# Kernel tuning notes

Measured on AMD Instinct MI355X. Metric: run time of the kernel, lower is better.

The kernel has to match this reference:

```python
import jax, jax.numpy as jnp
import numpy as np

N_NODES = 50000


def setup_inputs() -> dict:
    key = jax.random.key(0)
    k1, k2, k3, k4, k5 = jax.random.split(key, 5)
    feature = jax.random.normal(k1, (N_NODES, 128), dtype=jnp.float32)
    src = jax.random.randint(k2, (1600000,), 0, N_NODES, dtype=jnp.int32)
    dst = jax.random.randint(k3, (1600000,), 0, N_NODES, dtype=jnp.int32)
    W = jax.random.normal(k4, (128, 128), dtype=jnp.float32) * (1.0 / np.sqrt(128))
    b = jax.random.normal(k5, (128,), dtype=jnp.float32) * 0.01
    return {"feature": feature, "src": src, "dst": dst, "W": W, "b": b}


def reference(feature, src, dst, W, b):
    # DGL update_all(copy_src('h','m'), sum('m','h')):
    # for each edge (u -> v): message m = h[u]; node v accumulates sum of incoming messages.
    msgs = feature[src]  # [E, F] gather
    h = jax.ops.segment_sum(msgs, dst, num_segments=N_NODES)  # [N, F] scatter-add
    # nn.Linear(in_feats, out_feats): h @ W.T + b
    return h @ W.T + b
```

## Files before the change

### kernel.cpp

```cpp
#include <hip/hip_runtime.h>

#define F      128
#define RSH    5
#define RNODES 32
#define NBUCK  1563
#define CB     1280
#define CH     4096
#define OVCAP  65536
#define G_PART 391

typedef __attribute__((ext_vector_type(8))) short short8;
typedef __attribute__((ext_vector_type(4))) float f32x4;

__device__ inline short f2bf(float f) {
  unsigned u = __float_as_uint(f);
  u += 0x7fff + ((u >> 16) & 1);
  return (short)(u >> 16);
}
__device__ inline float bf2f(unsigned short u) {
  return __uint_as_float((unsigned)u << 16);
}

__global__ __launch_bounds__(512) void k_fused(
    const float* __restrict__ X, const float* __restrict__ W,
    const int* __restrict__ src, const int* __restrict__ dst,
    unsigned short* __restrict__ Yb,
    unsigned* __restrict__ pk, unsigned* __restrict__ gcur,
    unsigned* __restrict__ ovcnt, unsigned long long* __restrict__ ovlist,
    int N, int E, int nTiles) {
  __shared__ unsigned smem[CH + 3 * NBUCK];
  const int t = threadIdx.x;

  if (blockIdx.x < G_PART) {
    unsigned* lpk   = smem;
    unsigned* cnt   = smem + CH;
    unsigned* offs  = cnt + NBUCK;
    unsigned* cur   = offs + NBUCK;
    const int nchunk = (E + CH - 1) / CH;

    for (int c = blockIdx.x; c < nchunk; c += G_PART) {
      const int e0   = c * CH;
      const int ecnt = min(CH, E - e0);

      for (int i = t; i < NBUCK; i += 512) cnt[i] = 0;
      __syncthreads();

      for (int i = t; i < ecnt; i += 512)
        atomicAdd(&cnt[(unsigned)dst[e0 + i] >> RSH], 1u);
      __syncthreads();

      unsigned lv0, lv1, lv2, lv3;
      {
        const int i0 = t * 4;
        lv0 = (i0 + 0 < NBUCK) ? cnt[i0 + 0] : 0;
        lv1 = (i0 + 1 < NBUCK) ? cnt[i0 + 1] : 0;
        lv2 = (i0 + 2 < NBUCK) ? cnt[i0 + 2] : 0;
        lv3 = (i0 + 3 < NBUCK) ? cnt[i0 + 3] : 0;
      }
      cur[t] = lv0 + lv1 + lv2 + lv3;
      __syncthreads();
      for (int d2 = 1; d2 < 512; d2 <<= 1) {
        const unsigned add = (t >= d2) ? cur[t - d2] : 0;
        __syncthreads();
        cur[t] += add;
        __syncthreads();
      }
      unsigned ebase = (t > 0) ? cur[t - 1] : 0;
      __syncthreads();
      {
        const int i0 = t * 4;
        if (i0 + 0 < NBUCK) { offs[i0 + 0] = ebase; cur[i0 + 0] = ebase; ebase += lv0; }
        if (i0 + 1 < NBUCK) { offs[i0 + 1] = ebase; cur[i0 + 1] = ebase; ebase += lv1; }
        if (i0 + 2 < NBUCK) { offs[i0 + 2] = ebase; cur[i0 + 2] = ebase; ebase += lv2; }
        if (i0 + 3 < NBUCK) { offs[i0 + 3] = ebase; cur[i0 + 3] = ebase; ebase += lv3; }
      }
      __syncthreads();

      for (int i = t; i < ecnt; i += 512) {
        const unsigned d = (unsigned)dst[e0 + i];
        const unsigned b = d >> RSH;
        const unsigned p = atomicAdd(&cur[b], 1u);
        lpk[p] = (unsigned)src[e0 + i] | ((d & (RNODES - 1)) << 16) | (b << 21);
      }
      __syncthreads();

      for (int i = t; i < NBUCK; i += 512) {
        const unsigned c0 = cnt[i];
        if (c0 > 0) cnt[i] = (unsigned)i * CB + atomicAdd(&gcur[i], c0);
      }
      __syncthreads();

      for (int p = t; p < ecnt; p += 512) {
        const unsigned v = lpk[p];
        const unsigned b = v >> 21;
        const unsigned idx = cnt[b] + ((unsigned)p - offs[b]);
        if (idx < (b + 1) * (unsigned)CB) {
          pk[idx] = v & 0x1FFFFFu;
        } else {
          const unsigned o = atomicAdd(ovcnt, 1u);
          if (o < OVCAP) {
            const unsigned s  = v & 0xFFFFu;
            const unsigned dl = (v >> 16) & (RNODES - 1);
            ovlist[o] = ((unsigned long long)(b * RNODES + dl) << 32) | s;
          }
        }
      }
      __syncthreads();
    }
  } else {
    short* Wp = (short*)smem;
    for (int fid = t; fid < 2048; fid += 512) {
      const int lane = fid & 63;
      const int c    = (fid >> 6) & 3;
      const int jt   = fid >> 8;
      const int j    = jt * 16 + (lane & 15);
      const int k0   = c * 32 + (lane >> 4) * 8;
      short8 s;
      #pragma unroll
      for (int i = 0; i < 8; ++i) s[i] = f2bf(W[j * F + k0 + i]);
      *reinterpret_cast<short8*>(Wp + fid * 8) = s;
    }
    __syncthreads();

    const int lane = t & 63;
    const int tile = (blockIdx.x - G_PART) * 8 + (t >> 6);
    if (tile >= nTiles) return;
    const int row0 = tile * 16;
    const int r    = row0 + (lane & 15);
    const int k0   = (lane >> 4) * 8;

    short8 a[4];
    #pragma unroll
    for (int c = 0; c < 4; ++c) {
      if (r < N) {
        const float* p = X + (size_t)r * F + c * 32 + k0;
        const float4 x0 = *reinterpret_cast<const float4*>(p);
        const float4 x1 = *reinterpret_cast<const float4*>(p + 4);
        a[c][0] = f2bf(x0.x); a[c][1] = f2bf(x0.y);
        a[c][2] = f2bf(x0.z); a[c][3] = f2bf(x0.w);
        a[c][4] = f2bf(x1.x); a[c][5] = f2bf(x1.y);
        a[c][6] = f2bf(x1.z); a[c][7] = f2bf(x1.w);
      } else {
        #pragma unroll
        for (int i = 0; i < 8; ++i) a[c][i] = 0;
      }
    }

    #pragma unroll
    for (int jt = 0; jt < 8; ++jt) {
      f32x4 acc = {0.f, 0.f, 0.f, 0.f};
      #pragma unroll
      for (int c = 0; c < 4; ++c) {
        const short8 bfrag = *reinterpret_cast<const short8*>(
            Wp + ((jt * 4 + c) * 64 + lane) * 8);
        acc = __builtin_amdgcn_mfma_f32_16x16x32_bf16(a[c], bfrag, acc, 0, 0, 0);
      }
      const int col   = jt * 16 + (lane & 15);
      const int rbase = row0 + (lane >> 4) * 4;
      #pragma unroll
      for (int reg = 0; reg < 4; ++reg)
        if (rbase + reg < N)
          Yb[(size_t)(rbase + reg) * F + col] = (unsigned short)f2bf(acc[reg]);
    }
  }
}

__global__ __launch_bounds__(512) void k_reduce2(
    const unsigned short* __restrict__ Yb,
    const unsigned* __restrict__ pk,
    const unsigned* __restrict__ gcur,
    const float* __restrict__ b,
    float* __restrict__ out,
    int N) {
  __shared__ unsigned s_pk[CB];
  __shared__ unsigned short s_src[CB];
  __shared__ unsigned lcnt[RNODES], loffs[RNODES], lcur[RNODES];
  const int bkt = blockIdx.x % NBUCK;
  const int s   = blockIdx.x / NBUCK;
  const int t = threadIdx.x;
  const unsigned base = (unsigned)bkt * CB;
  const unsigned m = min(gcur[bkt], (unsigned)CB);

  for (unsigned i = t; i < m; i += 512) s_pk[i] = pk[base + i];
  if (t < RNODES) lcnt[t] = 0;
  __syncthreads();
  for (unsigned i = t; i < m; i += 512)
    atomicAdd(&lcnt[s_pk[i] >> 16], 1u);
  __syncthreads();
  if (t == 0) {
    unsigned r = 0;
    #pragma unroll
    for (int i = 0; i < RNODES; ++i) { loffs[i] = r; lcur[i] = r; r += lcnt[i]; }
  }
  __syncthreads();
  for (unsigned i = t; i < m; i += 512) {
    const unsigned v = s_pk[i];
    const unsigned p = atomicAdd(&lcur[v >> 16], 1u);
    s_src[p] = (unsigned short)(v & 0xFFFFu);
  }
  __syncthreads();

  const int lane = t & 63;
  const int g    = lane >> 4;
  const int q    = lane & 15;
  const int dl   = (t >> 6) * 4 + g;
  const int v    = bkt * RNODES + dl;
  const int deg  = (int)lcnt[dl];
  const int off  = (int)loffs[dl];
  const unsigned short* Yh = Yb + s * 64;

  float acc[4];
  #pragma unroll
  for (int j = 0; j < 4; ++j) acc[j] = 0.f;

  int k = 0;
  for (; k + 3 < deg; k += 4) {
    int sid[4];
    #pragma unroll
    for (int u = 0; u < 4; ++u) sid[u] = (int)s_src[off + k + u];
    ushort4 y[4];
    #pragma unroll
    for (int u = 0; u < 4; ++u)
      y[u] = *reinterpret_cast<const ushort4*>(
          Yh + (size_t)sid[u] * F + q * 4);
    acc[0] += (bf2f(y[0].x) + bf2f(y[1].x)) + (bf2f(y[2].x) + bf2f(y[3].x));
    acc[1] += (bf2f(y[0].y) + bf2f(y[1].y)) + (bf2f(y[2].y) + bf2f(y[3].y));
    acc[2] += (bf2f(y[0].z) + bf2f(y[1].z)) + (bf2f(y[2].z) + bf2f(y[3].z));
    acc[3] += (bf2f(y[0].w) + bf2f(y[1].w)) + (bf2f(y[2].w) + bf2f(y[3].w));
  }
  for (; k < deg; ++k) {
    const int s0 = (int)s_src[off + k];
    const ushort4 y = *reinterpret_cast<const ushort4*>(
        Yh + (size_t)s0 * F + q * 4);
    acc[0] += bf2f(y.x); acc[1] += bf2f(y.y);
    acc[2] += bf2f(y.z); acc[3] += bf2f(y.w);
  }

  if (v < N) {
    const int j = s * 64 + q * 4;
    const float4 bb = *reinterpret_cast<const float4*>(b + j);
    float4 o = make_float4(acc[0] + bb.x, acc[1] + bb.y,
                           acc[2] + bb.z, acc[3] + bb.w);
    *reinterpret_cast<float4*>(out + (size_t)v * F + j) = o;
  }
}

__global__ __launch_bounds__(256) void k_overflow(
    const unsigned* __restrict__ ovcnt,
    const unsigned long long* __restrict__ ovlist,
    const unsigned short* __restrict__ Yb,
    float* __restrict__ out, int N) {
  const unsigned n = min(*ovcnt, (unsigned)OVCAP);
  const int lane = threadIdx.x & 63;
  const int w  = (int)((blockIdx.x * blockDim.x + threadIdx.x) >> 6);
  const int nw = (int)((gridDim.x * blockDim.x) >> 6);
  for (unsigned i = w; i < n; i += nw) {
    const unsigned long long e = ovlist[i];
    const unsigned s = (unsigned)(e & 0xFFFFFFFFu);
    const unsigned d = (unsigned)(e >> 32);
    const float x0 = bf2f(Yb[(size_t)s * F + lane * 2]);
    const float x1 = bf2f(Yb[(size_t)s * F + lane * 2 + 1]);
    unsafeAtomicAdd(&out[(size_t)d * F + lane * 2],     x0);
    unsafeAtomicAdd(&out[(size_t)d * F + lane * 2 + 1], x1);
  }
}

extern "C" void kernel_launch(void* const* d_in, const int* in_sizes, int n_in,
                              void* d_out, int out_size, void* d_ws, size_t ws_size,
                              hipStream_t stream) {
  const float* feat = (const float*)d_in[0];
  const int*   src  = (const int*)d_in[1];
  const int*   dst  = (const int*)d_in[2];
  const float* W    = (const float*)d_in[3];
  const float* b    = (const float*)d_in[4];
  float*       out  = (float*)d_out;

  const int N = in_sizes[0] / F;
  const int E = in_sizes[1];

  char* w = (char*)d_ws;
  auto alloc = [&](size_t bytes) {
    char* p = w; w += (bytes + 255) & ~(size_t)255; return p;
  };
  unsigned short*     Yb      = (unsigned short*)alloc((size_t)N * F * 2);
  unsigned*           pk      = (unsigned*)alloc((size_t)NBUCK * CB * 4);
  unsigned*           gcur    = (unsigned*)alloc((size_t)(NBUCK + 1) * 4);
  unsigned*           ovcnt   = gcur + NBUCK;
  unsigned long long* ovlist  = (unsigned long long*)alloc((size_t)OVCAP * 8);

  hipMemsetAsync(gcur, 0, (size_t)(NBUCK + 1) * 4, stream);

  const int nTiles = (N + 15) / 16;
  const int gGemm  = (nTiles + 7) / 8;
  k_fused<<<G_PART + gGemm, 512, 0, stream>>>(
      feat, W, src, dst, Yb, pk, gcur, ovcnt, ovlist, N, E, nTiles);

  k_reduce2<<<2 * NBUCK, 512, 0, stream>>>(Yb, pk, gcur, b, out, N);

  k_overflow<<<16, 256, 0, stream>>>(ovcnt, ovlist, Yb, out, N);
}
```

Before: 80.62 us.

## Split edge bucketing into two-pass radix partition by coarse then fine buckets

Replaces the single-pass 1563-bucket partition with a two-level radix scatter. First, 49 coarse buckets of 1024 nodes each are filled in 8K-edge chunks. A new kernel then splits each coarse bucket into 32 fine buckets for the reducer. This removes the per-chunk 1563-entry prefix scan and the scattered writes to many small buckets, giving more coalesced global writes. The cost is an extra pass over the packed edges and one more kernel launch, and the fixed coarse capacity (5 sub-blocks of 8192) could overflow into the slow path.

```diff
diff --git a/kernel.cpp b/kernel.cpp
--- a/kernel.cpp
+++ b/kernel.cpp
@@ -1,13 +1,17 @@
 #include <hip/hip_runtime.h>
 
 #define F      128
-#define RSH    5
 #define RNODES 32
 #define NBUCK  1563
 #define CB     1280
-#define CH     4096
 #define OVCAP  65536
-#define G_PART 391
+
+#define CHA    8192
+#define NCB    49
+#define CCAP   34304
+#define G_PA   196
+#define CHB    8192
+#define NSUB   5
 
 typedef __attribute__((ext_vector_type(8))) short short8;
 typedef __attribute__((ext_vector_type(4))) float f32x4;
@@ -21,87 +25,64 @@
   return __uint_as_float((unsigned)u << 16);
 }
 
-__global__ __launch_bounds__(512) void k_fused(
+__global__ __launch_bounds__(512) void k_fusedA(
     const float* __restrict__ X, const float* __restrict__ W,
     const int* __restrict__ src, const int* __restrict__ dst,
     unsigned short* __restrict__ Yb,
-    unsigned* __restrict__ pk, unsigned* __restrict__ gcur,
+    unsigned* __restrict__ cpk, unsigned* __restrict__ ccur,
     unsigned* __restrict__ ovcnt, unsigned long long* __restrict__ ovlist,
     int N, int E, int nTiles) {
-  __shared__ unsigned smem[CH + 3 * NBUCK];
+  __shared__ unsigned smem[CHA + 4 * 64];
   const int t = threadIdx.x;
 
-  if (blockIdx.x < G_PART) {
+  if (blockIdx.x < G_PA) {
     unsigned* lpk   = smem;
-    unsigned* cnt   = smem + CH;
-    unsigned* offs  = cnt + NBUCK;
-    unsigned* cur   = offs + NBUCK;
-    const int nchunk = (E + CH - 1) / CH;
-
-    for (int c = blockIdx.x; c < nchunk; c += G_PART) {
-      const int e0   = c * CH;
-      const int ecnt = min(CH, E - e0);
-
-      for (int i = t; i < NBUCK; i += 512) cnt[i] = 0;
+    unsigned* cnt   = smem + CHA;
+    unsigned* offs  = cnt + 64;
+    unsigned* cur   = offs + 64;
+    unsigned* gbase = cur + 64;
+    const int nchunkA = (E + CHA - 1) / CHA;
+
+    for (int c = blockIdx.x; c < nchunkA; c += G_PA) {
+      const int e0   = c * CHA;
+      const int ecnt = min(CHA, E - e0);
+
+      if (t < NCB) cnt[t] = 0;
       __syncthreads();
 
       for (int i = t; i < ecnt; i += 512)
-        atomicAdd(&cnt[(unsigned)dst[e0 + i] >> RSH], 1u);
-      __syncthreads();
-
-      unsigned lv0, lv1, lv2, lv3;
-      {
-        const int i0 = t * 4;
-        lv0 = (i0 + 0 < NBUCK) ? cnt[i0 + 0] : 0;
-        lv1 = (i0 + 1 < NBUCK) ? cnt[i0 + 1] : 0;
-        lv2 = (i0 + 2 < NBUCK) ? cnt[i0 + 2] : 0;
-        lv3 = (i0 + 3 < NBUCK) ? cnt[i0 + 3] : 0;
-      }
-      cur[t] = lv0 + lv1 + lv2 + lv3;
-      __syncthreads();
-      for (int d2 = 1; d2 < 512; d2 <<= 1) {
-        const unsigned add = (t >= d2) ? cur[t - d2] : 0;
-        __syncthreads();
-        cur[t] += add;
-        __syncthreads();
-      }
-      unsigned ebase = (t > 0) ? cur[t - 1] : 0;
-      __syncthreads();
-      {
-        const int i0 = t * 4;
-        if (i0 + 0 < NBUCK) { offs[i0 + 0] = ebase; cur[i0 + 0] = ebase; ebase += lv0; }
-        if (i0 + 1 < NBUCK) { offs[i0 + 1] = ebase; cur[i0 + 1] = ebase; ebase += lv1; }
-        if (i0 + 2 < NBUCK) { offs[i0 + 2] = ebase; cur[i0 + 2] = ebase; ebase += lv2; }
-        if (i0 + 3 < NBUCK) { offs[i0 + 3] = ebase; cur[i0 + 3] = ebase; ebase += lv3; }
+        atomicAdd(&cnt[(unsigned)dst[e0 + i] >> 10], 1u);
+      __syncthreads();
+
+      if (t == 0) {
+        unsigned r = 0;
+        for (int i = 0; i < NCB; ++i) { offs[i] = r; cur[i] = r; r += cnt[i]; }
       }
       __syncthreads();
 
       for (int i = t; i < ecnt; i += 512) {
-        const unsigned d = (unsigned)dst[e0 + i];
-        const unsigned b = d >> RSH;
-        const unsigned p = atomicAdd(&cur[b], 1u);
-        lpk[p] = (unsigned)src[e0 + i] | ((d & (RNODES - 1)) << 16) | (b << 21);
-      }
-      __syncthreads();
-
-      for (int i = t; i < NBUCK; i += 512) {
-        const unsigned c0 = cnt[i];
-        if (c0 > 0) cnt[i] = (unsigned)i * CB + atomicAdd(&gcur[i], c0);
-      }
+        const unsigned d  = (unsigned)dst[e0 + i];
+        const unsigned cb = d >> 10;
+        const unsigned p  = atomicAdd(&cur[cb], 1u);
+        lpk[p] = (unsigned)src[e0 + i] | ((d & 1023u) << 16) | (cb << 26);
+      }
+      __syncthreads();
+
+      if (t < NCB && cnt[t] > 0)
+        gbase[t] = (unsigned)t * CCAP + atomicAdd(&ccur[t], cnt[t]);
       __syncthreads();
 
       for (int p = t; p < ecnt; p += 512) {
-        const unsigned v = lpk[p];
-        const unsigned b = v >> 21;
-        const unsigned idx = cnt[b] + ((unsigned)p - offs[b]);
-        if (idx < (b + 1) * (unsigned)CB) {
-          pk[idx] = v & 0x1FFFFFu;
+        const unsigned v  = lpk[p];
+        const unsigned cb = v >> 26;
+        const unsigned idx = gbase[cb] + ((unsigned)p - offs[cb]);
+        if (idx < (cb + 1) * (unsigned)CCAP) {
+          cpk[idx] = v & 0x03FFFFFFu;
         } else {
           const unsigned o = atomicAdd(ovcnt, 1u);
           if (o < OVCAP) {
-            const unsigned s  = v & 0xFFFFu;
-            const unsigned dl = (v >> 16) & (RNODES - 1);
-            ovlist[o] = ((unsigned long long)(b * RNODES + dl) << 32) | s;
+            const unsigned node = cb * 1024u + ((v >> 16) & 1023u);
+            ovlist[o] = ((unsigned long long)node << 32) | (v & 0xFFFFu);
           }
         }
       }
@@ -123,7 +104,7 @@
     __syncthreads();
 
     const int lane = t & 63;
-    const int tile = (blockIdx.x - G_PART) * 8 + (t >> 6);
+    const int tile = (blockIdx.x - G_PA) * 8 + (t >> 6);
     if (tile >= nTiles) return;
     const int row0 = tile * 16;
     const int r    = row0 + (lane & 15);
@@ -161,6 +142,67 @@
       for (int reg = 0; reg < 4; ++reg)
         if (rbase + reg < N)
           Yb[(size_t)(rbase + reg) * F + col] = (unsigned short)f2bf(acc[reg]);
+    }
+  }
+}
+
+__global__ __launch_bounds__(512) void k_partB(
+    const unsigned* __restrict__ cpk, const unsigned* __restrict__ ccur,
+    unsigned* __restrict__ pk, unsigned* __restrict__ gcur,
+    unsigned* __restrict__ ovcnt, unsigned long long* __restrict__ ovlist) {
+  const int cb  = blockIdx.x / NSUB;
+  const int sub = blockIdx.x % NSUB;
+  const int mA  = (int)min(ccur[cb], (unsigned)CCAP);
+  const int e0  = sub * CHB;
+  const int ecnt = min(CHB, mA - e0);
+  if (ecnt <= 0) return;
+
+  __shared__ unsigned lpk[CHB];
+  __shared__ unsigned cnt[32], offs[32], cur[32], gbase[32];
+  const int t = threadIdx.x;
+  const unsigned base = (unsigned)cb * CCAP + e0;
+
+  if (t < 32) cnt[t] = 0;
+  __syncthreads();
+
+  for (int i = t; i < ecnt; i += 512)
+    atomicAdd(&cnt[(cpk[base + i] >> 21) & 31u], 1u);
+  __syncthreads();
+
+  if (t == 0) {
+    unsigned r = 0;
+    #pragma unroll
+    for (int i = 0; i < 32; ++i) { offs[i] = r; cur[i] = r; r += cnt[i]; }
+  }
+  __syncthreads();
+
+  for (int i = t; i < ecnt; i += 512) {
+    const unsigned v  = cpk[base + i];
+    const unsigned fb = (v >> 21) & 31u;
+    const unsigned p  = atomicAdd(&cur[fb], 1u);
+    lpk[p] = v;
+  }
+  __syncthreads();
+
+  if (t < 32 && cnt[t] > 0) {
+    const unsigned gfb = (unsigned)cb * 32 + t;
+    gbase[t] = gfb * CB + atomicAdd(&gcur[gfb], cnt[t]);
+  }
+  __syncthreads();
+
+  for (int p = t; p < ecnt; p += 512) {
+    const unsigned v   = lpk[p];
+    const unsigned fb  = (v >> 21) & 31u;
+    const unsigned gfb = (unsigned)cb * 32 + fb;
+    const unsigned idx = gbase[fb] + ((unsigned)p - offs[fb]);
+    if (idx < (gfb + 1) * (unsigned)CB) {
+      pk[idx] = v & 0x001FFFFFu;
+    } else {
+      const unsigned o = atomicAdd(ovcnt, 1u);
+      if (o < OVCAP) {
+        const unsigned node = (unsigned)cb * 1024u + ((v >> 16) & 1023u);
+        ovlist[o] = ((unsigned long long)node << 32) | (v & 0xFFFFu);
+      }
     }
   }
 }
@@ -283,17 +325,22 @@
     char* p = w; w += (bytes + 255) & ~(size_t)255; return p;
   };
   unsigned short*     Yb      = (unsigned short*)alloc((size_t)N * F * 2);
+  unsigned*           cpk     = (unsigned*)alloc((size_t)NCB * CCAP * 4);
   unsigned*           pk      = (unsigned*)alloc((size_t)NBUCK * CB * 4);
-  unsigned*           gcur    = (unsigned*)alloc((size_t)(NBUCK + 1) * 4);
+  unsigned*           gcur    = (unsigned*)alloc((size_t)(NBUCK + 1 + NCB) * 4);
   unsigned*           ovcnt   = gcur + NBUCK;
+  unsigned*           ccur    = ovcnt + 1;
   unsigned long long* ovlist  = (unsigned long long*)alloc((size_t)OVCAP * 8);
 
-  hipMemsetAsync(gcur, 0, (size_t)(NBUCK + 1) * 4, stream);
+  hipMemsetAsync(gcur, 0, (size_t)(NBUCK + 1 + NCB) * 4, stream);
 
   const int nTiles = (N + 15) / 16;
   const int gGemm  = (nTiles + 7) / 8;
-  k_fused<<<G_PART + gGemm, 512, 0, stream>>>(
-      feat, W, src, dst, Yb, pk, gcur, ovcnt, ovlist, N, E, nTiles);
+  k_fusedA<<<G_PA + gGemm, 512, 0, stream>>>(
+      feat, W, src, dst, Yb, cpk, ccur, ovcnt, ovlist, N, E, nTiles);
+
+  k_partB<<<NCB * NSUB, 512, 0, stream>>>(
+      cpk, ccur, pk, gcur, ovcnt, ovlist);
 
   k_reduce2<<<2 * NBUCK, 512, 0, stream>>>(Yb, pk, gcur, b, out, N);
 
```

Result: slower. 92.56 us (+14.8%).
